# Performance work log

Measured on AMD Instinct MI355X. Metric: run time of the kernel, lower is better.

Reference implementation:

```python
import jax, jax.numpy as jnp
import numpy as np

B, S, D, H = 4, 2048, 1024, 16
DEPTH = D // H  # 64


def setup_inputs() -> dict:
    key = jax.random.key(0)
    ks = jax.random.split(key, 7)
    scale = 1.0 / np.sqrt(D)
    return {
        "x": jax.random.normal(ks[0], (B, S, D), dtype=jnp.float32),
        "y": jax.random.normal(ks[1], (B, S, D), dtype=jnp.float32),
        "bias": jax.random.normal(ks[2], (1, 1, S, S), dtype=jnp.float32),
        "Wq": jax.random.normal(ks[3], (D, D), dtype=jnp.float32) * scale,
        "Wk": jax.random.normal(ks[4], (D, D), dtype=jnp.float32) * scale,
        "Wv": jax.random.normal(ks[5], (D, D), dtype=jnp.float32) * scale,
        "Wo": jax.random.normal(ks[6], (D, D), dtype=jnp.float32) * scale,
    }


def _split_heads(t):
    # [B, S, D] -> [B, H, S, depth]
    b, s, _ = t.shape
    return t.reshape(b, s, H, DEPTH).transpose(0, 2, 1, 3)


def reference(x, y, bias, Wq, Wk, Wv, Wo):
    # nn.Linear(bias=False): out = in @ W.T
    q = _split_heads(x @ Wq.T) * (DEPTH ** -0.5)  # [B,H,Sx,depth]
    k = _split_heads(y @ Wk.T)                    # [B,H,Sy,depth]
    v = _split_heads(y @ Wv.T)                    # [B,H,Sy,depth]
    logits = jnp.einsum('bhqd,bhkd->bhqk', q, k) + bias  # [B,H,Sx,Sy]
    weights = jax.nn.softmax(logits, axis=-1)
    attn = jnp.einsum('bhqk,bhkd->bhqd', weights, v)     # [B,H,Sx,depth]
    # combine heads: [B,H,Sx,depth] -> [B,Sx,D]
    attn = attn.transpose(0, 2, 1, 3).reshape(x.shape[0], x.shape[1], D)
    return attn @ Wo.T
```

## Files before the change

kernel.cpp:

```cpp
#include <hip/hip_runtime.h>
#include <hip/hip_bf16.h>

#define Bn 4
#define Sn 2048
#define Dn 1024
#define Hn 16
#define DEPTHn 64

typedef __attribute__((ext_vector_type(8))) short short8;
typedef __attribute__((ext_vector_type(4))) float float4v;

#define LOG2E 1.44269504088896340736f
#define C16   23.083120654223414f

__device__ __forceinline__ void load_lds16(const void* g, void* l) {
  __builtin_amdgcn_global_load_lds(
      (const __attribute__((address_space(1))) unsigned int*)g,
      (__attribute__((address_space(3))) unsigned int*)l, 16, 0, 0);
}

__global__ __launch_bounds__(256) void cast_xy(const float* __restrict__ x,
                                               const float* __restrict__ y,
                                               __hip_bfloat16* __restrict__ out) {
  int i = blockIdx.x * blockDim.x + threadIdx.x;
  const float* src = (i >> 20) ? y : x;
  int j = i & 1048575;
  float v[8];
  *(float4*)&v[0] = ((const float4*)src)[2 * j];
  *(float4*)&v[4] = ((const float4*)src)[2 * j + 1];
  union { __hip_bfloat16 h[8]; short8 s; } u;
#pragma unroll
  for (int k = 0; k < 8; ++k) u.h[k] = __float2bfloat16(v[k]);
  ((short8*)out)[i] = u.s;
}

__global__ __launch_bounds__(256) void cast_w(const float* __restrict__ wq,
                                              const float* __restrict__ wk,
                                              const float* __restrict__ wv,
                                              const float* __restrict__ wo,
                                              __hip_bfloat16* __restrict__ out) {
  int i = blockIdx.x * blockDim.x + threadIdx.x;
  int which = i >> 17, j = i & 131071;
  const float* src = (which == 0) ? wq : (which == 1) ? wk : (which == 2) ? wv : wo;
  float scale = (which == 0) ? 0.125f : 1.0f;
  float v[8];
  *(float4*)&v[0] = ((const float4*)src)[2 * j];
  *(float4*)&v[4] = ((const float4*)src)[2 * j + 1];
  union { __hip_bfloat16 h[8]; short8 s; } u;
#pragma unroll
  for (int k = 0; k < 8; ++k) u.h[k] = __float2bfloat16(v[k] * scale);
  ((short8*)out)[i] = u.s;
}

__global__ __launch_bounds__(256) void rearrange_bias(const float* __restrict__ in,
                                                      float* __restrict__ out) {
  int t = blockIdx.x * blockDim.x + threadIdx.x;
  int r = t & 3, lane = (t >> 2) & 63, wm = (t >> 8) & 15;
  int jti = (t >> 12) & 15, qb = (t >> 16) & 7;
  int wave = wm >> 2, mt = wm & 3, quad = lane >> 4, l16 = lane & 15;
  int row = qb * 256 + wave * 64 + mt * 16 + quad * 4 + r;
  const float* src = in + (size_t)row * Sn + jti * 128 + l16;
  float4v o0, o1;
#pragma unroll
  for (int j = 0; j < 4; ++j) o0[j] = fmaf(src[j * 16], LOG2E, -C16);
#pragma unroll
  for (int j = 0; j < 4; ++j) o1[j] = fmaf(src[(j + 4) * 16], LOG2E, -C16);
  ((float4v*)out)[t * 2] = o0;
  ((float4v*)out)[t * 2 + 1] = o1;
}

__global__ __launch_bounds__(256) void gemm_qkv(const __hip_bfloat16* __restrict__ Xb,
                                                const __hip_bfloat16* __restrict__ Yb,
                                                const __hip_bfloat16* __restrict__ Wqkv,
                                                __hip_bfloat16* __restrict__ Qb,
                                                __hip_bfloat16* __restrict__ Kb,
                                                __hip_bfloat16* __restrict__ Vtb) {
  constexpr int Kdim = 1024;
  __shared__ char pool[128 * 129 * 2];
  __hip_bfloat16* As = (__hip_bfloat16*)pool;
  __hip_bfloat16* Bs = As + 128 * 64;
  __hip_bfloat16* Sg = (__hip_bfloat16*)pool;

  const int tid = threadIdx.x;
  const int wave = tid >> 6, lane = tid & 63;
  const int quad = lane >> 4, l16 = lane & 15;
  const int bm = blockIdx.x, bn = blockIdx.y;
  const int sel = bn >> 3;
  const int wm = (wave & 1) * 64, wn = (wave >> 1) * 64;
  const __hip_bfloat16* A = (sel == 0) ? Xb : Yb;

  const __hip_bfloat16* aptr[4];
  const __hip_bfloat16* bptr[4];
#pragma unroll
  for (int i = 0; i < 4; ++i) {
    int c = wave * 4 + i;
    aptr[i] = A + (size_t)(bm * 128 + c * 8 + (lane >> 3)) * Kdim + (lane & 7) * 8;
    bptr[i] = Wqkv + (size_t)(bn * 128 + c * 8 + (lane >> 3)) * Kdim + (lane & 7) * 8;
  }

  float4v acc[4][4];
#pragma unroll
  for (int i = 0; i < 4; ++i)
#pragma unroll
    for (int j = 0; j < 4; ++j) acc[i][j] = (float4v){0.f, 0.f, 0.f, 0.f};

  for (int kt = 0; kt < Kdim / 64; ++kt) {
    __syncthreads();
#pragma unroll
    for (int i = 0; i < 4; ++i) {
      int c = wave * 4 + i;
      load_lds16(aptr[i] + kt * 64, &As[c * 512]);
      load_lds16(bptr[i] + kt * 64, &Bs[c * 512]);
    }
    __syncthreads();
#pragma unroll
    for (int ks = 0; ks < 2; ++ks) {
      short8 af[4], bf[4];
#pragma unroll
      for (int i = 0; i < 4; ++i)
        af[i] = *(const short8*)&As[(wm + i * 16 + l16) * 64 + ks * 32 + quad * 8];
#pragma unroll
      for (int j = 0; j < 4; ++j)
        bf[j] = *(const short8*)&Bs[(wn + j * 16 + l16) * 64 + ks * 32 + quad * 8];
#pragma unroll
      for (int i = 0; i < 4; ++i)
#pragma unroll
        for (int j = 0; j < 4; ++j)
          acc[i][j] = __builtin_amdgcn_mfma_f32_16x16x32_bf16(af[i], bf[j], acc[i][j], 0, 0, 0);
    }
  }

  const int b = bm >> 4;
  if (sel < 2) {
    __hip_bfloat16* dst = (sel == 0) ? Qb : Kb;
    const int nbase = (bn & 7) * 128;
#pragma unroll
    for (int i = 0; i < 4; ++i)
#pragma unroll
      for (int j = 0; j < 4; ++j)
#pragma unroll
        for (int r = 0; r < 4; ++r) {
          int row = bm * 128 + wm + i * 16 + quad * 4 + r;
          int col = nbase + wn + j * 16 + l16;
          int s = row & 2047, h = col >> 6, d = col & 63;
          int d2 = d ^ ((s & 7) << 3);
          dst[(((size_t)b * Hn + h) * Sn + s) * DEPTHn + d2] = __float2bfloat16(acc[i][j][r]);
        }
  } else {
    __syncthreads();
#pragma unroll
    for (int i = 0; i < 4; ++i)
#pragma unroll
      for (int j = 0; j < 4; ++j)
#pragma unroll
        for (int r = 0; r < 4; ++r) {
          int row = wm + i * 16 + quad * 4 + r;
          int col = wn + j * 16 + l16;
          Sg[row * 129 + col] = __float2bfloat16(acc[i][j][r]);
        }
    __syncthreads();
    const int s_tile = (bm & 15) * 128;
#pragma unroll
    for (int iter = 0; iter < 8; ++iter) {
      int id = iter * 256 + tid;
      int chunk = id & 15, lcol = id >> 4;
      int hg = (bn - 16) * 2 + (lcol >> 6), d = lcol & 63;
      int c = chunk ^ (d & 7);
      union { __hip_bfloat16 h[8]; short8 s8; } pu;
#pragma unroll
      for (int i = 0; i < 8; ++i) pu.h[i] = Sg[(i * 16 + c) * 129 + lcol];
      *(short8*)&Vtb[(((size_t)b * Hn + hg) * DEPTHn + d) * Sn + s_tile + chunk * 8] = pu.s8;
    }
  }
}

__global__ __launch_bounds__(256) void gemm_out(const __hip_bfloat16* __restrict__ A,
                                                const __hip_bfloat16* __restrict__ B,
                                                float* __restrict__ Cf) {
  constexpr int Kdim = 1024;
  __shared__ __hip_bfloat16 As[128 * 64];
  __shared__ __hip_bfloat16 Bs[128 * 64];
  const int tid = threadIdx.x;
  const int wave = tid >> 6, lane = tid & 63;
  const int quad = lane >> 4, l16 = lane & 15;
  const int bm = blockIdx.x, bn = blockIdx.y;
  const int wm = (wave & 1) * 64, wn = (wave >> 1) * 64;

  const __hip_bfloat16* aptr[4];
  const __hip_bfloat16* bptr[4];
#pragma unroll
  for (int i = 0; i < 4; ++i) {
    int c = wave * 4 + i;
    aptr[i] = A + (size_t)(bm * 128 + c * 8 + (lane >> 3)) * Kdim + (lane & 7) * 8;
    bptr[i] = B + (size_t)(bn * 128 + c * 8 + (lane >> 3)) * Kdim + (lane & 7) * 8;
  }

  float4v acc[4][4];
#pragma unroll
  for (int i = 0; i < 4; ++i)
#pragma unroll
    for (int j = 0; j < 4; ++j) acc[i][j] = (float4v){0.f, 0.f, 0.f, 0.f};

  for (int kt = 0; kt < Kdim / 64; ++kt) {
    __syncthreads();
#pragma unroll
    for (int i = 0; i < 4; ++i) {
      int c = wave * 4 + i;
      load_lds16(aptr[i] + kt * 64, &As[c * 512]);
      load_lds16(bptr[i] + kt * 64, &Bs[c * 512]);
    }
    __syncthreads();
#pragma unroll
    for (int ks = 0; ks < 2; ++ks) {
      short8 af[4], bf[4];
#pragma unroll
      for (int i = 0; i < 4; ++i)
        af[i] = *(const short8*)&As[(wm + i * 16 + l16) * 64 + ks * 32 + quad * 8];
#pragma unroll
      for (int j = 0; j < 4; ++j)
        bf[j] = *(const short8*)&Bs[(wn + j * 16 + l16) * 64 + ks * 32 + quad * 8];
#pragma unroll
      for (int i = 0; i < 4; ++i)
#pragma unroll
        for (int j = 0; j < 4; ++j)
          acc[i][j] = __builtin_amdgcn_mfma_f32_16x16x32_bf16(af[i], bf[j], acc[i][j], 0, 0, 0);
    }
  }
#pragma unroll
  for (int i = 0; i < 4; ++i)
#pragma unroll
    for (int j = 0; j < 4; ++j)
#pragma unroll
      for (int r = 0; r < 4; ++r) {
        int row = bm * 128 + wm + i * 16 + quad * 4 + r;
        int col = bn * 128 + wn + j * 16 + l16;
        Cf[(size_t)row * 1024 + col] = acc[i][j][r];
      }
}

__global__ __launch_bounds__(256, 2) void flash_attn(const __hip_bfloat16* __restrict__ Q,
                                                     const __hip_bfloat16* __restrict__ Kh,
                                                     const __hip_bfloat16* __restrict__ Vt,
                                                     const float* __restrict__ biasR,
                                                     __hip_bfloat16* __restrict__ O) {
  __shared__ __hip_bfloat16 Ks[128 * 64];
  __shared__ __hip_bfloat16 Vts[64 * 128];
  __shared__ __hip_bfloat16 Ps[4][32 * 128];
  const int tid = threadIdx.x;
  const int wave = tid >> 6, lane = tid & 63;
  const int quad = lane >> 4, l16 = lane & 15;
  const int swk = (l16 & 7) << 3;
  const int lin = blockIdx.x;
  const int bh = (lin & 7) * 8 + ((lin >> 3) & 7);
  const int qb = lin >> 6;
  const int q0 = qb * 256;
  const __hip_bfloat16* Qp = Q + (size_t)bh * Sn * DEPTHn;
  const __hip_bfloat16* Kp = Kh + (size_t)bh * Sn * DEPTHn;
  const __hip_bfloat16* Vp = Vt + (size_t)bh * DEPTHn * Sn;

  short8 qf[4][2];
#pragma unroll
  for (int mt = 0; mt < 4; ++mt)
#pragma unroll
    for (int ks = 0; ks < 2; ++ks)
      qf[mt][ks] = *(const short8*)&Qp[(size_t)(q0 + wave * 64 + mt * 16 + l16) * 64 +
                                       ((ks * 32 + quad * 8) ^ swk)];

  float l_i[4][4];
  float4v oacc[4][4];
#pragma unroll
  for (int mt = 0; mt < 4; ++mt)
#pragma unroll
    for (int r = 0; r < 4; ++r) l_i[mt][r] = 0.f;
#pragma unroll
  for (int mt = 0; mt < 4; ++mt)
#pragma unroll
    for (int nt = 0; nt < 4; ++nt) oacc[mt][nt] = (float4v){0.f, 0.f, 0.f, 0.f};

  const int koff = (lane >> 3) * 64 + (lane & 7) * 8;
  const int voff = (lane >> 4) * Sn + l16 * 8;

  for (int jti = 0; jti < 16; ++jti) {
    const int j0 = jti * 128;
    __syncthreads();
#pragma unroll
    for (int i = 0; i < 4; ++i) {
      int c = wave * 4 + i;
      load_lds16(Kp + (size_t)(j0 + c * 8) * 64 + koff, &Ks[c * 512]);
      load_lds16(Vp + (size_t)(c * 4) * Sn + j0 + voff, &Vts[c * 512]);
    }
    __syncthreads();

#pragma unroll
    for (int mtp = 0; mtp < 2; ++mtp) {
      float4v sacc[2][8];
#pragma unroll
      for (int m2 = 0; m2 < 2; ++m2)
#pragma unroll
        for (int jt = 0; jt < 8; ++jt) sacc[m2][jt] = (float4v){0.f, 0.f, 0.f, 0.f};
#pragma unroll
      for (int ks = 0; ks < 2; ++ks) {
        short8 kf[8];
#pragma unroll
        for (int jt = 0; jt < 8; ++jt)
          kf[jt] = *(const short8*)&Ks[(jt * 16 + l16) * 64 + ((ks * 32 + quad * 8) ^ swk)];
#pragma unroll
        for (int m2 = 0; m2 < 2; ++m2)
#pragma unroll
          for (int jt = 0; jt < 8; ++jt)
            sacc[m2][jt] = __builtin_amdgcn_mfma_f32_16x16x32_bf16(qf[mtp * 2 + m2][ks], kf[jt],
                                                                   sacc[m2][jt], 0, 0, 0);
      }

#pragma unroll
      for (int m2 = 0; m2 < 2; ++m2) {
        const int mt = mtp * 2 + m2;
        const float4v* bp = (const float4v*)biasR +
                            ((((size_t)(qb * 16 + jti) * 16 + wave * 4 + mt) * 64 + lane) << 3);
#pragma unroll
        for (int r = 0; r < 4; ++r) {
          float4v b0 = bp[r * 2], b1 = bp[r * 2 + 1];
          float ls = 0.f;
          union { __hip_bfloat16 h[8]; short8 s8; } pu;
#pragma unroll
          for (int jt = 0; jt < 8; ++jt) {
            float bb = (jt < 4) ? b0[jt] : b1[jt - 4];
            float p = __builtin_amdgcn_exp2f(fmaf(sacc[m2][jt][r], LOG2E, bb));
            ls += p;
            pu.h[jt] = __float2bfloat16(p);
          }
          l_i[mt][r] += ls;
          const int prow = m2 * 16 + quad * 4 + r;
          *(short8*)&Ps[wave][prow * 128 + ((l16 ^ (prow & 7)) << 3)] = pu.s8;
        }
      }

#pragma unroll
      for (int ks = 0; ks < 4; ++ks) {
        short8 vf[4];
#pragma unroll
        for (int nt = 0; nt < 4; ++nt)
          vf[nt] = *(const short8*)&Vts[(nt * 16 + l16) * 128 + ((ks * 32 + quad * 8) ^ swk)];
#pragma unroll
        for (int m2 = 0; m2 < 2; ++m2) {
          short8 pf = *(const short8*)&Ps[wave][(m2 * 16 + l16) * 128 +
                                               ((ks * 32 + quad * 8) ^ swk)];
#pragma unroll
          for (int nt = 0; nt < 4; ++nt)
            oacc[mtp * 2 + m2][nt] =
                __builtin_amdgcn_mfma_f32_16x16x32_bf16(pf, vf[nt], oacc[mtp * 2 + m2][nt], 0, 0, 0);
        }
      }
    }
  }

  const int b = bh >> 4, h = bh & 15;
#pragma unroll
  for (int mt = 0; mt < 4; ++mt) {
    float inv[4];
#pragma unroll
    for (int r = 0; r < 4; ++r) {
      float l = l_i[mt][r];
#pragma unroll
      for (int off = 1; off < 16; off <<= 1) l += __shfl_xor(l, off, 64);
      inv[r] = __builtin_amdgcn_rcpf(l);
    }
#pragma unroll
    for (int nt = 0; nt < 4; ++nt)
#pragma unroll
      for (int r = 0; r < 4; ++r) {
        int s = q0 + wave * 64 + mt * 16 + quad * 4 + r;
        int d = nt * 16 + l16;
        O[((size_t)b * Sn + s) * Dn + h * 64 + d] = __float2bfloat16(oacc[mt][nt][r] * inv[r]);
      }
  }
}

extern "C" void kernel_launch(void* const* d_in, const int* in_sizes, int n_in,
                              void* d_out, int out_size, void* d_ws, size_t ws_size,
                              hipStream_t stream) {
  const float* x = (const float*)d_in[0];
  const float* y = (const float*)d_in[1];
  const float* bias = (const float*)d_in[2];
  const float* Wq = (const float*)d_in[3];
  const float* Wk = (const float*)d_in[4];
  const float* Wv = (const float*)d_in[5];
  const float* Wo = (const float*)d_in[6];
  float* out = (float*)d_out;

  const size_t SZ_XY = (size_t)Bn * Sn * Dn * 2;
  const size_t SZ_W = (size_t)Dn * Dn * 2;
  const size_t SZ_BIASF = (size_t)Sn * Sn * 4;

  char* p = (char*)d_ws;
  __hip_bfloat16* xb = (__hip_bfloat16*)p;      p += SZ_XY;
  __hip_bfloat16* yb = (__hip_bfloat16*)p;      p += SZ_XY;
  __hip_bfloat16* wqkv = (__hip_bfloat16*)p;    p += 3 * SZ_W;
  __hip_bfloat16* wob = (__hip_bfloat16*)p;     p += SZ_W;
  float* biasR = (float*)p;                     p += SZ_BIASF;
  __hip_bfloat16* Qb = (__hip_bfloat16*)p;      p += SZ_XY;
  __hip_bfloat16* Kb = (__hip_bfloat16*)p;      p += SZ_XY;
  __hip_bfloat16* Vtb = (__hip_bfloat16*)p;     p += SZ_XY;
  __hip_bfloat16* attnb = (__hip_bfloat16*)p;   p += SZ_XY;

  cast_xy<<<2 * 1048576 / 256, 256, 0, stream>>>(x, y, xb);
  cast_w<<<(4 * Dn * Dn / 8) / 256, 256, 0, stream>>>(Wq, Wk, Wv, Wo, wqkv);
  rearrange_bias<<<(Sn * Sn / 8) / 256, 256, 0, stream>>>(bias, biasR);

  gemm_qkv<<<dim3(64, 24), 256, 0, stream>>>(xb, yb, wqkv, Qb, Kb, Vtb);

  flash_attn<<<512, 256, 0, stream>>>(Qb, Kb, Vtb, biasR, attnb);

  gemm_out<<<dim3(64, 8), 256, 0, stream>>>(attnb, wob, out);
}
```

Measured before the change: 395.7 us.

## Double-buffer K tiles and prefetch next K/V during flash attention compute

The flash attention loop now double-buffers the K tile in LDS and issues the next tile's K loads before computing the current scores. V is single-buffered and reloaded after the end-of-iteration barrier. The P buffer shrinks to one 16-row tile per wave, interleaving softmax and PV per m2, which frees LDS. Bias loads are hoisted into a register array and prefetched, and s_setprio raises priority around the MFMA phases. The goal is to overlap global loads with MFMA work and cut barrier stalls, at the cost of more registers and careful sync ordering. The Ps reuse and the mid-iteration barrier depend on wave synchronization being correct.

Measured after the change: 523.5 us. +32.3%, slower.

```diff
diff --git a/kernel.cpp b/kernel.cpp
--- a/kernel.cpp
+++ b/kernel.cpp
@@ -243,9 +243,9 @@
                                                      const __hip_bfloat16* __restrict__ Vt,
                                                      const float* __restrict__ biasR,
                                                      __hip_bfloat16* __restrict__ O) {
-  __shared__ __hip_bfloat16 Ks[128 * 64];
+  __shared__ __hip_bfloat16 Ks[2][128 * 64];
   __shared__ __hip_bfloat16 Vts[64 * 128];
-  __shared__ __hip_bfloat16 Ps[4][32 * 128];
+  __shared__ __hip_bfloat16 Ps[4][16 * 128];
   const int tid = threadIdx.x;
   const int wave = tid >> 6, lane = tid & 63;
   const int quad = lane >> 4, l16 = lane & 15;
@@ -280,16 +280,24 @@
   const int koff = (lane >> 3) * 64 + (lane & 7) * 8;
   const int voff = (lane >> 4) * Sn + l16 * 8;
 
+#pragma unroll
+  for (int i = 0; i < 4; ++i) {
+    int c = wave * 4 + i;
+    load_lds16(Kp + (size_t)(c * 8) * 64 + koff, &Ks[0][c * 512]);
+    load_lds16(Vp + (size_t)(c * 4) * Sn + voff, &Vts[c * 512]);
+  }
+  __syncthreads();
+
   for (int jti = 0; jti < 16; ++jti) {
-    const int j0 = jti * 128;
-    __syncthreads();
-#pragma unroll
-    for (int i = 0; i < 4; ++i) {
-      int c = wave * 4 + i;
-      load_lds16(Kp + (size_t)(j0 + c * 8) * 64 + koff, &Ks[c * 512]);
-      load_lds16(Vp + (size_t)(c * 4) * Sn + j0 + voff, &Vts[c * 512]);
-    }
-    __syncthreads();
+    const int cur = jti & 1;
+    if (jti < 15) {
+      const int j0n = (jti + 1) * 128;
+#pragma unroll
+      for (int i = 0; i < 4; ++i) {
+        int c = wave * 4 + i;
+        load_lds16(Kp + (size_t)(j0n + c * 8) * 64 + koff, &Ks[cur ^ 1][c * 512]);
+      }
+    }
 
 #pragma unroll
     for (int mtp = 0; mtp < 2; ++mtp) {
@@ -298,12 +306,13 @@
       for (int m2 = 0; m2 < 2; ++m2)
 #pragma unroll
         for (int jt = 0; jt < 8; ++jt) sacc[m2][jt] = (float4v){0.f, 0.f, 0.f, 0.f};
+      __builtin_amdgcn_s_setprio(1);
 #pragma unroll
       for (int ks = 0; ks < 2; ++ks) {
         short8 kf[8];
 #pragma unroll
         for (int jt = 0; jt < 8; ++jt)
-          kf[jt] = *(const short8*)&Ks[(jt * 16 + l16) * 64 + ((ks * 32 + quad * 8) ^ swk)];
+          kf[jt] = *(const short8*)&Ks[cur][(jt * 16 + l16) * 64 + ((ks * 32 + quad * 8) ^ swk)];
 #pragma unroll
         for (int m2 = 0; m2 < 2; ++m2)
 #pragma unroll
@@ -311,45 +320,61 @@
             sacc[m2][jt] = __builtin_amdgcn_mfma_f32_16x16x32_bf16(qf[mtp * 2 + m2][ks], kf[jt],
                                                                    sacc[m2][jt], 0, 0, 0);
       }
+      __builtin_amdgcn_s_setprio(0);
+      if (mtp == 0) __syncthreads();
+
+      const float4v* bpb = (const float4v*)biasR +
+                           ((((size_t)(qb * 16 + jti) * 16 + wave * 4 + mtp * 2) * 64 + lane) << 3);
+      float4v bb[8];
+#pragma unroll
+      for (int t = 0; t < 8; ++t) bb[t] = bpb[t];
 
 #pragma unroll
       for (int m2 = 0; m2 < 2; ++m2) {
         const int mt = mtp * 2 + m2;
-        const float4v* bp = (const float4v*)biasR +
-                            ((((size_t)(qb * 16 + jti) * 16 + wave * 4 + mt) * 64 + lane) << 3);
 #pragma unroll
         for (int r = 0; r < 4; ++r) {
-          float4v b0 = bp[r * 2], b1 = bp[r * 2 + 1];
           float ls = 0.f;
           union { __hip_bfloat16 h[8]; short8 s8; } pu;
+          float4v B0 = bb[r * 2], B1 = bb[r * 2 + 1];
 #pragma unroll
           for (int jt = 0; jt < 8; ++jt) {
-            float bb = (jt < 4) ? b0[jt] : b1[jt - 4];
-            float p = __builtin_amdgcn_exp2f(fmaf(sacc[m2][jt][r], LOG2E, bb));
+            float bv = (jt < 4) ? B0[jt] : B1[jt - 4];
+            float p = __builtin_amdgcn_exp2f(fmaf(sacc[m2][jt][r], LOG2E, bv));
             ls += p;
             pu.h[jt] = __float2bfloat16(p);
           }
           l_i[mt][r] += ls;
-          const int prow = m2 * 16 + quad * 4 + r;
+          const int prow = quad * 4 + r;
           *(short8*)&Ps[wave][prow * 128 + ((l16 ^ (prow & 7)) << 3)] = pu.s8;
         }
-      }
-
-#pragma unroll
-      for (int ks = 0; ks < 4; ++ks) {
-        short8 vf[4];
-#pragma unroll
-        for (int nt = 0; nt < 4; ++nt)
-          vf[nt] = *(const short8*)&Vts[(nt * 16 + l16) * 128 + ((ks * 32 + quad * 8) ^ swk)];
-#pragma unroll
-        for (int m2 = 0; m2 < 2; ++m2) {
-          short8 pf = *(const short8*)&Ps[wave][(m2 * 16 + l16) * 128 +
-                                               ((ks * 32 + quad * 8) ^ swk)];
+        if (m2 == 0) {
+#pragma unroll
+          for (int t = 0; t < 8; ++t) bb[t] = bpb[512 + t];
+        }
+        __builtin_amdgcn_s_setprio(1);
+#pragma unroll
+        for (int ks = 0; ks < 4; ++ks) {
+          short8 vf[4];
 #pragma unroll
           for (int nt = 0; nt < 4; ++nt)
-            oacc[mtp * 2 + m2][nt] =
-                __builtin_amdgcn_mfma_f32_16x16x32_bf16(pf, vf[nt], oacc[mtp * 2 + m2][nt], 0, 0, 0);
+            vf[nt] = *(const short8*)&Vts[(nt * 16 + l16) * 128 + ((ks * 32 + quad * 8) ^ swk)];
+          short8 pf = *(const short8*)&Ps[wave][l16 * 128 + ((ks * 32 + quad * 8) ^ swk)];
+#pragma unroll
+          for (int nt = 0; nt < 4; ++nt)
+            oacc[mt][nt] =
+                __builtin_amdgcn_mfma_f32_16x16x32_bf16(pf, vf[nt], oacc[mt][nt], 0, 0, 0);
         }
+        __builtin_amdgcn_s_setprio(0);
+      }
+    }
+    __syncthreads();
+    if (jti < 15) {
+      const int j0n = (jti + 1) * 128;
+#pragma unroll
+      for (int i = 0; i < 4; ++i) {
+        int c = wave * 4 + i;
+        load_lds16(Vp + (size_t)(c * 4) * Sn + j0n + voff, &Vts[c * 512]);
       }
     }
   }
```
